# Kernel optimization log

Measured on AMD Instinct MI355X. Metric: run time of the kernel, lower is better.

Reference implementation:

```python
import jax, jax.numpy as jnp
import numpy as np

N = 2048
INPUT_DIM = 256
OUTPUT_DIM = 512
NUM_HEADS = 8
HEAD_DIM = OUTPUT_DIM // NUM_HEADS


def _lin_init(key, fan_in, fan_out):
    # torch nn.Linear default init: U(-1/sqrt(fan_in), 1/sqrt(fan_in))
    kw, kb = jax.random.split(key)
    bound = 1.0 / np.sqrt(fan_in)
    W = jax.random.uniform(kw, (fan_in, fan_out), jnp.float32, -bound, bound)
    b = jax.random.uniform(kb, (fan_out,), jnp.float32, -bound, bound)
    return W, b


def setup_inputs() -> dict:
    key = jax.random.key(0)
    ks = jax.random.split(key, 12)
    x = jax.random.normal(ks[0], (N, INPUT_DIM), jnp.float32)
    rel_pos = jax.random.normal(ks[1], (N, 2), jnp.float32)
    rel_vel = jax.random.normal(ks[2], (N, 1), jnp.float32)
    rel_angle = jax.random.normal(ks[3], (N, 1), jnp.float32)
    Wq, bq = _lin_init(ks[4], INPUT_DIM, OUTPUT_DIM)
    Wk, bk = _lin_init(ks[5], INPUT_DIM, OUTPUT_DIM)
    Wv, bv = _lin_init(ks[6], INPUT_DIM, OUTPUT_DIM)
    Wsb1, bsb1 = _lin_init(ks[7], 2, HEAD_DIM)
    Wsb2, bsb2 = _lin_init(ks[8], HEAD_DIM, 1)
    Wmg1, bmg1 = _lin_init(ks[9], 2, HEAD_DIM)
    Wmg2, bmg2 = _lin_init(ks[10], HEAD_DIM, 1)
    Wo, bo = _lin_init(ks[11], OUTPUT_DIM, 1)
    return dict(x=x, rel_pos=rel_pos, rel_vel=rel_vel, rel_angle=rel_angle,
                Wq=Wq, bq=bq, Wk=Wk, bk=bk, Wv=Wv, bv=bv,
                Wsb1=Wsb1, bsb1=bsb1, Wsb2=Wsb2, bsb2=bsb2,
                Wmg1=Wmg1, bmg1=bmg1, Wmg2=Wmg2, bmg2=bmg2,
                Wo=Wo, bo=bo)


def reference(x, rel_pos, rel_vel, rel_angle,
              Wq, bq, Wk, bk, Wv, bv,
              Wsb1, bsb1, Wsb2, bsb2,
              Wmg1, bmg1, Wmg2, bmg2,
              Wo, bo):
    n = x.shape[0]
    Q = (x @ Wq + bq).reshape(n, NUM_HEADS, HEAD_DIM)
    K = (x @ Wk + bk).reshape(n, NUM_HEADS, HEAD_DIM)
    V = (x @ Wv + bv).reshape(n, NUM_HEADS, HEAD_DIM)

    # scores[q, k, h] = <Q[q,h], K[k,h]> / sqrt(head_dim)
    scores = jnp.einsum('qhd,khd->qkh', Q, K) / np.sqrt(HEAD_DIM).astype(np.float32)

    # spatial bias: per-query scalar, broadcast over keys and heads
    sb = (jax.nn.relu(rel_pos @ Wsb1 + bsb1) @ Wsb2 + bsb2)  # (N, 1)
    scores = scores + sb[:, :, None]  # (N,1,1) broadcast -> (N,N,H)

    # softmax over key dim (dim=1)
    attention = jax.nn.softmax(scores, axis=1)

    # motion gate: per-key scalar in (0,1)
    motion_feat = jnp.concatenate([rel_vel, rel_angle], axis=-1)  # (N, 2)
    mg = jax.nn.sigmoid(jax.nn.relu(motion_feat @ Wmg1 + bmg1) @ Wmg2 + bmg2)  # (N, 1)
    attention = attention * mg[None, :, 0, None]  # (1,N,1) broadcast

    # weighted sum over keys without materializing (N,N,H,D)
    out = jnp.einsum('qkh,khd->qhd', attention, V).reshape(n, OUTPUT_DIM)
    out = out @ Wo + bo  # (N, 1)
    return out[:, 0]
```

## Files before the change

kernel.cpp:

```cpp
#include <hip/hip_runtime.h>
#include <hip/hip_bf16.h>

constexpr int N    = 2048;
constexpr int IN   = 256;
constexpr int OUT  = 512;
constexpr int NH   = 8;
constexpr int HD   = 64;
constexpr int NQK  = 1024;
constexpr int NC   = 8;
constexpr int KPB  = N / NC;
constexpr int KT   = KPB / 16;

typedef __bf16    bf16x8 __attribute__((ext_vector_type(8)));
typedef __bf16    bf16x4 __attribute__((ext_vector_type(4)));
typedef _Float16  f16x8  __attribute__((ext_vector_type(8)));
typedef float     f32x4  __attribute__((ext_vector_type(4)));

#if __has_builtin(__builtin_amdgcn_exp2f)
#define EXP2(x) __builtin_amdgcn_exp2f(x)
#else
#define EXP2(x) exp2f(x)
#endif

#define QSCALE (0.125f * 1.44269504088896f)

__global__ __launch_bounds__(256)
void prep_all(const float* __restrict__ x,
              const float* __restrict__ Wq, const float* __restrict__ Wk,
              const float* __restrict__ Wv, const float* __restrict__ bv,
              const float* __restrict__ Wo,
              __bf16* __restrict__ Xhi, __bf16* __restrict__ Xlo,
              __bf16* __restrict__ WThi, __bf16* __restrict__ WTlo,
              float* __restrict__ Wvo, float* __restrict__ bvo) {
    __shared__ float smem[32 * 33];
    const int b = blockIdx.x;
    const int tid = threadIdx.x;

    if (b < 512) {
        const size_t i4 = ((size_t)b * 256 + tid) * 4;
        const float4 v = *(const float4*)(x + i4);
        const float vv[4] = {v.x, v.y, v.z, v.w};
        bf16x4 hi, lo;
        #pragma unroll
        for (int j = 0; j < 4; j++) {
            const __bf16 h = (__bf16)vv[j];
            hi[j] = h;
            lo[j] = (__bf16)(vv[j] - (float)h);
        }
        *(bf16x4*)(Xhi + i4) = hi;
        *(bf16x4*)(Xlo + i4) = lo;
    } else if (b < 768) {
        const int tb = b - 512;
        const int k0 = (tb & 7) * 32;
        const int n0 = (tb >> 3) * 32;
        const float* W = (n0 < OUT) ? Wq : Wk;
        const int nc = (n0 < OUT) ? n0 : n0 - OUT;
        {
            const int row = tid >> 3;
            const int c4  = (tid & 7) * 4;
            const float4 v = *(const float4*)(W + (size_t)(k0 + row) * OUT + nc + c4);
            smem[row * 33 + c4 + 0] = v.x;
            smem[row * 33 + c4 + 1] = v.y;
            smem[row * 33 + c4 + 2] = v.z;
            smem[row * 33 + c4 + 3] = v.w;
        }
        __syncthreads();
        {
            const int nrow = tid >> 3;
            const int k4   = (tid & 7) * 4;
            bf16x4 hi, lo;
            #pragma unroll
            for (int j = 0; j < 4; j++) {
                const float v = smem[(k4 + j) * 33 + nrow];
                const __bf16 h = (__bf16)v;
                hi[j] = h;
                lo[j] = (__bf16)(v - (float)h);
            }
            const size_t off = (size_t)(n0 + nrow) * IN + k0 + k4;
            *(bf16x4*)(WThi + off) = hi;
            *(bf16x4*)(WTlo + off) = lo;
        }
    } else {
        float* wo_s = smem;
        wo_s[tid]       = Wo[tid];
        wo_s[tid + 256] = Wo[tid + 256];
        __syncthreads();
        const int i = (b - 768) * 32 + (tid >> 3);
        const int h = tid & 7;
        const float* wr = Wv + (size_t)i * OUT + h * HD;
        float s = 0.f;
        #pragma unroll
        for (int d = 0; d < HD; d += 4) {
            const float4 v = *(const float4*)(wr + d);
            s += v.x * wo_s[h * HD + d + 0] + v.y * wo_s[h * HD + d + 1]
               + v.z * wo_s[h * HD + d + 2] + v.w * wo_s[h * HD + d + 3];
        }
        Wvo[i * NH + h] = s;
        if (b == 768 && tid < NH) {
            float sb = 0.f;
            #pragma unroll
            for (int d = 0; d < HD; d++)
                sb += bv[tid * HD + d] * wo_s[tid * HD + d];
            bvo[tid] = sb;
        }
    }
}

__global__ __launch_bounds__(256)
void gemm_qk(const __bf16* __restrict__ Xhi, const __bf16* __restrict__ Xlo,
             const __bf16* __restrict__ WThi, const __bf16* __restrict__ WTlo,
             const float* __restrict__ bq, const float* __restrict__ bk,
             _Float16* __restrict__ Qh, _Float16* __restrict__ Kh) {
    __shared__ _Float16 stage[32 * 132];
    const int tid  = threadIdx.x;
    const int lane = tid & 63;
    const int wave = tid >> 6;
    const int row16 = lane & 15;
    const int quad  = lane >> 4;
    const int mb = blockIdx.y * 32;
    const int nb0 = blockIdx.x * 128;
    const int nb = nb0 + wave * 32;

    const size_t ar[2] = {(size_t)(mb + row16) * IN, (size_t)(mb + 16 + row16) * IN};
    const size_t br[2] = {(size_t)(nb + row16) * IN, (size_t)(nb + 16 + row16) * IN};

    f32x4 acc[2][2] = {};
    for (int k0 = 0; k0 < IN; k0 += 32) {
        const int ko = k0 + quad * 8;
        bf16x8 ah[2], al[2], bh[2], bl[2];
        #pragma unroll
        for (int t = 0; t < 2; t++) {
            ah[t] = *(const bf16x8*)(Xhi + ar[t] + ko);
            al[t] = *(const bf16x8*)(Xlo + ar[t] + ko);
            bh[t] = *(const bf16x8*)(WThi + br[t] + ko);
            bl[t] = *(const bf16x8*)(WTlo + br[t] + ko);
        }
        #pragma unroll
        for (int mt = 0; mt < 2; mt++)
            #pragma unroll
            for (int nt = 0; nt < 2; nt++) {
                acc[mt][nt] = __builtin_amdgcn_mfma_f32_16x16x32_bf16(ah[mt], bh[nt], acc[mt][nt], 0, 0, 0);
                acc[mt][nt] = __builtin_amdgcn_mfma_f32_16x16x32_bf16(ah[mt], bl[nt], acc[mt][nt], 0, 0, 0);
                acc[mt][nt] = __builtin_amdgcn_mfma_f32_16x16x32_bf16(al[mt], bh[nt], acc[mt][nt], 0, 0, 0);
            }
    }

    const bool isQ = (nb0 < OUT);
    const float scale = isQ ? QSCALE : 1.0f;
    #pragma unroll
    for (int mt = 0; mt < 2; mt++)
        #pragma unroll
        for (int nt = 0; nt < 2; nt++) {
            const int nl = wave * 32 + nt * 16 + row16;
            const int np = nb0 + nl;
            const int nq = isQ ? np : np - OUT;
            const float bias = isQ ? bq[nq] : bk[nq];
            #pragma unroll
            for (int r = 0; r < 4; r++) {
                const int ml = mt * 16 + quad * 4 + r;
                stage[ml * 132 + nl] = (_Float16)((acc[mt][nt][r] + bias) * scale);
            }
        }
    __syncthreads();

    _Float16* dst = isQ ? Qh : Kh;
    const int r2   = tid >> 2;
    const int cidx = tid & 3;
    const int hl   = r2 >> 5;
    const int m    = r2 & 31;
    const int nqh  = (isQ ? nb0 : nb0 - OUT) + hl * 64;
    const int h    = nqh >> 6;
    const size_t goff = ((size_t)h * N + mb + m) * HD + cidx * 16;
    const int soff = m * 132 + hl * 64 + cidx * 16;
    *(f16x8*)(dst + goff)     = *(const f16x8*)(&stage[soff]);
    *(f16x8*)(dst + goff + 8) = *(const f16x8*)(&stage[soff + 8]);
}

__global__ __launch_bounds__(256)
void compute_vpm(const float* __restrict__ x, const float* __restrict__ rel_vel,
                 const float* __restrict__ rel_angle,
                 const float* __restrict__ Wmg1, const float* __restrict__ bmg1,
                 const float* __restrict__ Wmg2, const float* __restrict__ bmg2,
                 const float* __restrict__ Wvo, const float* __restrict__ bvo,
                 float* __restrict__ vpmT) {
    __shared__ float wvo_s[IN * NH];
    const int tid = threadIdx.x;
    #pragma unroll
    for (int i = 0; i < 8; i++) wvo_s[tid + 256 * i] = Wvo[tid + 256 * i];
    __syncthreads();

    const int k = blockIdx.x * 32 + (tid >> 3);
    const int h = tid & 7;

    const float m0 = rel_vel[k], m1 = rel_angle[k];
    float g = bmg2[0];
    #pragma unroll
    for (int j = 0; j < HD; j++) {
        float t = m0 * Wmg1[j] + m1 * Wmg1[HD + j] + bmg1[j];
        t = fmaxf(t, 0.f);
        g += t * Wmg2[j];
    }
    const float mg = 1.f / (1.f + __expf(-g));

    const float4* xr = (const float4*)(x + (size_t)k * IN);
    float a0 = 0.f, a1 = 0.f, a2 = 0.f, a3 = 0.f;
    #pragma unroll 4
    for (int i = 0; i < IN / 4; i++) {
        const float4 v = xr[i];
        a0 += v.x * wvo_s[(i * 4 + 0) * NH + h];
        a1 += v.y * wvo_s[(i * 4 + 1) * NH + h];
        a2 += v.z * wvo_s[(i * 4 + 2) * NH + h];
        a3 += v.w * wvo_s[(i * 4 + 3) * NH + h];
    }
    vpmT[h * N + k] = mg * (a0 + a1 + a2 + a3 + bvo[h]);
}

__global__ __launch_bounds__(256)
void attn_mfma(const _Float16* __restrict__ Qh, const _Float16* __restrict__ Kh,
               const float* __restrict__ vpmT,
               float* __restrict__ pnum, float* __restrict__ pden) {
    const int b = blockIdx.x;
    const int h = b & 7;
    const int r = b >> 3;
    const int c = r >> 3;
    const int qg = r & 7;
    const int lane = threadIdx.x & 63;
    const int wave = threadIdx.x >> 6;
    const int q0 = (qg * 4 + wave) * 64;
    const int row16 = lane & 15;
    const int quad  = lane >> 4;

    f16x8 Bq[4][2];
    #pragma unroll
    for (int qt = 0; qt < 4; qt++) {
        const size_t qoff = ((size_t)h * N + q0 + qt * 16 + row16) * HD + quad * 8;
        Bq[qt][0] = *(const f16x8*)(Qh + qoff);
        Bq[qt][1] = *(const f16x8*)(Qh + qoff + 32);
    }

    float num[4] = {}, den[4] = {};
    const int k0 = c * KPB;
    const size_t kbase = ((size_t)h * N + k0 + row16) * HD + quad * 8;
    const float* vp = vpmT + h * N + k0 + quad * 4;

    f16x8 A0 = *(const f16x8*)(Kh + kbase);
    f16x8 A1 = *(const f16x8*)(Kh + kbase + 32);
    f32x4 vv = *(const f32x4*)(vp);

    #pragma unroll
    for (int t = 0; t < KT; t++) {
        const int tn = (t + 1 < KT) ? t + 1 : t;
        const size_t ka = kbase + (size_t)tn * 16 * HD;
        const f16x8 nA0 = *(const f16x8*)(Kh + ka);
        const f16x8 nA1 = *(const f16x8*)(Kh + ka + 32);
        const f32x4 nvv = *(const f32x4*)(vp + tn * 16);

        #pragma unroll
        for (int qt = 0; qt < 4; qt++) {
            f32x4 s = {0.f, 0.f, 0.f, 0.f};
            s = __builtin_amdgcn_mfma_f32_16x16x32_f16(A0, Bq[qt][0], s, 0, 0, 0);
            s = __builtin_amdgcn_mfma_f32_16x16x32_f16(A1, Bq[qt][1], s, 0, 0, 0);
            #pragma unroll
            for (int r4 = 0; r4 < 4; r4++) {
                const float e = EXP2(s[r4]);
                num[qt] += e * vv[r4];
                den[qt] += e;
            }
        }
        A0 = nA0; A1 = nA1; vv = nvv;
    }

    #pragma unroll
    for (int qt = 0; qt < 4; qt++) {
        float n = num[qt], d = den[qt];
        n += __shfl_xor(n, 16, 64);  d += __shfl_xor(d, 16, 64);
        n += __shfl_xor(n, 32, 64);  d += __shfl_xor(d, 32, 64);
        if (quad == 0) {
            const int q = q0 + qt * 16 + row16;
            pnum[((size_t)c * NH + h) * N + q] = n;
            pden[((size_t)c * NH + h) * N + q] = d;
        }
    }
}

__global__ __launch_bounds__(64)
void finalize(const float* __restrict__ pnum, const float* __restrict__ pden,
              const float* __restrict__ bo, float* __restrict__ out) {
    const int q = blockIdx.x * 64 + threadIdx.x;
    float acc = bo[0];
    #pragma unroll
    for (int h = 0; h < NH; h++) {
        float num = 0.f, den = 0.f;
        #pragma unroll
        for (int ci = 0; ci < NC; ci++) {
            num += pnum[((size_t)ci * NH + h) * N + q];
            den += pden[((size_t)ci * NH + h) * N + q];
        }
        acc += num / den;
    }
    out[q] = acc;
}

extern "C" void kernel_launch(void* const* d_in, const int* in_sizes, int n_in,
                              void* d_out, int out_size, void* d_ws, size_t ws_size,
                              hipStream_t stream) {
    const float* x         = (const float*)d_in[0];
    const float* rel_vel   = (const float*)d_in[2];
    const float* rel_angle = (const float*)d_in[3];
    const float* Wq        = (const float*)d_in[4];
    const float* bq        = (const float*)d_in[5];
    const float* Wk        = (const float*)d_in[6];
    const float* bk        = (const float*)d_in[7];
    const float* Wv        = (const float*)d_in[8];
    const float* bv        = (const float*)d_in[9];
    const float* Wmg1      = (const float*)d_in[14];
    const float* bmg1      = (const float*)d_in[15];
    const float* Wmg2      = (const float*)d_in[16];
    const float* bmg2      = (const float*)d_in[17];
    const float* Wo        = (const float*)d_in[18];
    const float* bo        = (const float*)d_in[19];
    float* out = (float*)d_out;

    __bf16* Xhi  = (__bf16*)d_ws;
    __bf16* Xlo  = Xhi + (size_t)N * IN;
    __bf16* WThi = Xlo + (size_t)N * IN;
    __bf16* WTlo = WThi + (size_t)NQK * IN;
    _Float16* Qh = (_Float16*)(WTlo + (size_t)NQK * IN);
    _Float16* Kh = Qh + (size_t)NH * N * HD;
    float* fp    = (float*)(Kh + (size_t)NH * N * HD);
    float* Wvo   = fp;
    float* bvo   = Wvo + IN * NH;
    float* vpmT  = bvo + NH;
    float* pnum  = vpmT + NH * N;
    float* pden  = pnum + (size_t)NC * NH * N;

    hipLaunchKernelGGL(prep_all, dim3(776), dim3(256), 0, stream,
                       x, Wq, Wk, Wv, bv, Wo, Xhi, Xlo, WThi, WTlo, Wvo, bvo);
    hipLaunchKernelGGL(gemm_qk, dim3(NQK / 128, N / 32), dim3(256), 0, stream,
                       Xhi, Xlo, WThi, WTlo, bq, bk, Qh, Kh);
    hipLaunchKernelGGL(compute_vpm, dim3(N / 32), dim3(256), 0, stream,
                       x, rel_vel, rel_angle, Wmg1, bmg1, Wmg2, bmg2, Wvo, bvo, vpmT);
    hipLaunchKernelGGL(attn_mfma, dim3(512), dim3(256), 0, stream,
                       Qh, Kh, vpmT, pnum, pden);
    hipLaunchKernelGGL(finalize, dim3(N / 64), dim3(64), 0, stream, pnum, pden, bo, out);
}
```

Baseline: 147.5 us.

## Use single fp16 QK projection, merge vpm into gemm, split keys into more chunks

Replaces the split-bf16 (hi/lo, three MFMAs) QK projection with a single fp16 conversion and one f16 MFMA per tile, halving the conversion traffic and cutting matrix work to a third. Folds the compute_vpm kernel into the gemm launch as extra blocks to remove a kernel launch. Doubles the key-chunk count for attention so twice as many blocks run. This costs some precision in the Q/K scores and more partial results for finalize to reduce.

After: 136.5 us. 7.5% less time.

```diff
diff --git a/kernel.cpp b/kernel.cpp
--- a/kernel.cpp
+++ b/kernel.cpp
@@ -7,13 +7,12 @@
 constexpr int NH   = 8;
 constexpr int HD   = 64;
 constexpr int NQK  = 1024;
-constexpr int NC   = 8;
+constexpr int NC   = 16;
 constexpr int KPB  = N / NC;
 constexpr int KT   = KPB / 16;
 
-typedef __bf16    bf16x8 __attribute__((ext_vector_type(8)));
-typedef __bf16    bf16x4 __attribute__((ext_vector_type(4)));
 typedef _Float16  f16x8  __attribute__((ext_vector_type(8)));
+typedef _Float16  f16x4  __attribute__((ext_vector_type(4)));
 typedef float     f32x4  __attribute__((ext_vector_type(4)));
 
 #if __has_builtin(__builtin_amdgcn_exp2f)
@@ -29,8 +28,7 @@
               const float* __restrict__ Wq, const float* __restrict__ Wk,
               const float* __restrict__ Wv, const float* __restrict__ bv,
               const float* __restrict__ Wo,
-              __bf16* __restrict__ Xhi, __bf16* __restrict__ Xlo,
-              __bf16* __restrict__ WThi, __bf16* __restrict__ WTlo,
+              _Float16* __restrict__ X16, _Float16* __restrict__ WT,
               float* __restrict__ Wvo, float* __restrict__ bvo) {
     __shared__ float smem[32 * 33];
     const int b = blockIdx.x;
@@ -39,16 +37,10 @@
     if (b < 512) {
         const size_t i4 = ((size_t)b * 256 + tid) * 4;
         const float4 v = *(const float4*)(x + i4);
-        const float vv[4] = {v.x, v.y, v.z, v.w};
-        bf16x4 hi, lo;
-        #pragma unroll
-        for (int j = 0; j < 4; j++) {
-            const __bf16 h = (__bf16)vv[j];
-            hi[j] = h;
-            lo[j] = (__bf16)(vv[j] - (float)h);
-        }
-        *(bf16x4*)(Xhi + i4) = hi;
-        *(bf16x4*)(Xlo + i4) = lo;
+        f16x4 o;
+        o[0] = (_Float16)v.x; o[1] = (_Float16)v.y;
+        o[2] = (_Float16)v.z; o[3] = (_Float16)v.w;
+        *(f16x4*)(X16 + i4) = o;
     } else if (b < 768) {
         const int tb = b - 512;
         const int k0 = (tb & 7) * 32;
@@ -68,17 +60,11 @@
         {
             const int nrow = tid >> 3;
             const int k4   = (tid & 7) * 4;
-            bf16x4 hi, lo;
-            #pragma unroll
-            for (int j = 0; j < 4; j++) {
-                const float v = smem[(k4 + j) * 33 + nrow];
-                const __bf16 h = (__bf16)v;
-                hi[j] = h;
-                lo[j] = (__bf16)(v - (float)h);
-            }
-            const size_t off = (size_t)(n0 + nrow) * IN + k0 + k4;
-            *(bf16x4*)(WThi + off) = hi;
-            *(bf16x4*)(WTlo + off) = lo;
+            f16x4 o;
+            #pragma unroll
+            for (int j = 0; j < 4; j++)
+                o[j] = (_Float16)smem[(k4 + j) * 33 + nrow];
+            *(f16x4*)(WT + (size_t)(n0 + nrow) * IN + k0 + k4) = o;
         }
     } else {
         float* wo_s = smem;
@@ -107,19 +93,58 @@
 }
 
 __global__ __launch_bounds__(256)
-void gemm_qk(const __bf16* __restrict__ Xhi, const __bf16* __restrict__ Xlo,
-             const __bf16* __restrict__ WThi, const __bf16* __restrict__ WTlo,
-             const float* __restrict__ bq, const float* __restrict__ bk,
-             _Float16* __restrict__ Qh, _Float16* __restrict__ Kh) {
+void gemm_qk_vpm(const _Float16* __restrict__ X16, const _Float16* __restrict__ WT,
+                 const float* __restrict__ bq, const float* __restrict__ bk,
+                 _Float16* __restrict__ Qh, _Float16* __restrict__ Kh,
+                 const float* __restrict__ x, const float* __restrict__ rel_vel,
+                 const float* __restrict__ rel_angle,
+                 const float* __restrict__ Wmg1, const float* __restrict__ bmg1,
+                 const float* __restrict__ Wmg2, const float* __restrict__ bmg2,
+                 const float* __restrict__ Wvo, const float* __restrict__ bvo,
+                 float* __restrict__ vpmT) {
     __shared__ _Float16 stage[32 * 132];
-    const int tid  = threadIdx.x;
+    __shared__ float wvo_s[IN * NH];
+    const int tid = threadIdx.x;
+
+    if (blockIdx.x >= 512) {
+        #pragma unroll
+        for (int i = 0; i < 8; i++) wvo_s[tid + 256 * i] = Wvo[tid + 256 * i];
+        __syncthreads();
+
+        const int k = (blockIdx.x - 512) * 32 + (tid >> 3);
+        const int h = tid & 7;
+
+        const float m0 = rel_vel[k], m1 = rel_angle[k];
+        float g = bmg2[0];
+        #pragma unroll
+        for (int j = 0; j < HD; j++) {
+            float t = m0 * Wmg1[j] + m1 * Wmg1[HD + j] + bmg1[j];
+            t = fmaxf(t, 0.f);
+            g += t * Wmg2[j];
+        }
+        const float mg = 1.f / (1.f + __expf(-g));
+
+        const float4* xr = (const float4*)(x + (size_t)k * IN);
+        float a0 = 0.f, a1 = 0.f, a2 = 0.f, a3 = 0.f;
+        #pragma unroll 4
+        for (int i = 0; i < IN / 4; i++) {
+            const float4 v = xr[i];
+            a0 += v.x * wvo_s[(i * 4 + 0) * NH + h];
+            a1 += v.y * wvo_s[(i * 4 + 1) * NH + h];
+            a2 += v.z * wvo_s[(i * 4 + 2) * NH + h];
+            a3 += v.w * wvo_s[(i * 4 + 3) * NH + h];
+        }
+        vpmT[h * N + k] = mg * (a0 + a1 + a2 + a3 + bvo[h]);
+        return;
+    }
+
     const int lane = tid & 63;
     const int wave = tid >> 6;
     const int row16 = lane & 15;
     const int quad  = lane >> 4;
-    const int mb = blockIdx.y * 32;
-    const int nb0 = blockIdx.x * 128;
-    const int nb = nb0 + wave * 32;
+    const int nb0 = (blockIdx.x & 7) * 128;
+    const int mb  = (blockIdx.x >> 3) * 32;
+    const int nb  = nb0 + wave * 32;
 
     const size_t ar[2] = {(size_t)(mb + row16) * IN, (size_t)(mb + 16 + row16) * IN};
     const size_t br[2] = {(size_t)(nb + row16) * IN, (size_t)(nb + 16 + row16) * IN};
@@ -127,22 +152,17 @@
     f32x4 acc[2][2] = {};
     for (int k0 = 0; k0 < IN; k0 += 32) {
         const int ko = k0 + quad * 8;
-        bf16x8 ah[2], al[2], bh[2], bl[2];
+        f16x8 a[2], bf[2];
         #pragma unroll
         for (int t = 0; t < 2; t++) {
-            ah[t] = *(const bf16x8*)(Xhi + ar[t] + ko);
-            al[t] = *(const bf16x8*)(Xlo + ar[t] + ko);
-            bh[t] = *(const bf16x8*)(WThi + br[t] + ko);
-            bl[t] = *(const bf16x8*)(WTlo + br[t] + ko);
+            a[t]  = *(const f16x8*)(X16 + ar[t] + ko);
+            bf[t] = *(const f16x8*)(WT + br[t] + ko);
         }
         #pragma unroll
         for (int mt = 0; mt < 2; mt++)
             #pragma unroll
-            for (int nt = 0; nt < 2; nt++) {
-                acc[mt][nt] = __builtin_amdgcn_mfma_f32_16x16x32_bf16(ah[mt], bh[nt], acc[mt][nt], 0, 0, 0);
-                acc[mt][nt] = __builtin_amdgcn_mfma_f32_16x16x32_bf16(ah[mt], bl[nt], acc[mt][nt], 0, 0, 0);
-                acc[mt][nt] = __builtin_amdgcn_mfma_f32_16x16x32_bf16(al[mt], bh[nt], acc[mt][nt], 0, 0, 0);
-            }
+            for (int nt = 0; nt < 2; nt++)
+                acc[mt][nt] = __builtin_amdgcn_mfma_f32_16x16x32_f16(a[mt], bf[nt], acc[mt][nt], 0, 0, 0);
     }
 
     const bool isQ = (nb0 < OUT);
@@ -174,45 +194,6 @@
     const int soff = m * 132 + hl * 64 + cidx * 16;
     *(f16x8*)(dst + goff)     = *(const f16x8*)(&stage[soff]);
     *(f16x8*)(dst + goff + 8) = *(const f16x8*)(&stage[soff + 8]);
-}
-
-__global__ __launch_bounds__(256)
-void compute_vpm(const float* __restrict__ x, const float* __restrict__ rel_vel,
-                 const float* __restrict__ rel_angle,
-                 const float* __restrict__ Wmg1, const float* __restrict__ bmg1,
-                 const float* __restrict__ Wmg2, const float* __restrict__ bmg2,
-                 const float* __restrict__ Wvo, const float* __restrict__ bvo,
-                 float* __restrict__ vpmT) {
-    __shared__ float wvo_s[IN * NH];
-    const int tid = threadIdx.x;
-    #pragma unroll
-    for (int i = 0; i < 8; i++) wvo_s[tid + 256 * i] = Wvo[tid + 256 * i];
-    __syncthreads();
-
-    const int k = blockIdx.x * 32 + (tid >> 3);
-    const int h = tid & 7;
-
-    const float m0 = rel_vel[k], m1 = rel_angle[k];
-    float g = bmg2[0];
-    #pragma unroll
-    for (int j = 0; j < HD; j++) {
-        float t = m0 * Wmg1[j] + m1 * Wmg1[HD + j] + bmg1[j];
-        t = fmaxf(t, 0.f);
-        g += t * Wmg2[j];
-    }
-    const float mg = 1.f / (1.f + __expf(-g));
-
-    const float4* xr = (const float4*)(x + (size_t)k * IN);
-    float a0 = 0.f, a1 = 0.f, a2 = 0.f, a3 = 0.f;
-    #pragma unroll 4
-    for (int i = 0; i < IN / 4; i++) {
-        const float4 v = xr[i];
-        a0 += v.x * wvo_s[(i * 4 + 0) * NH + h];
-        a1 += v.y * wvo_s[(i * 4 + 1) * NH + h];
-        a2 += v.z * wvo_s[(i * 4 + 2) * NH + h];
-        a3 += v.w * wvo_s[(i * 4 + 3) * NH + h];
-    }
-    vpmT[h * N + k] = mg * (a0 + a1 + a2 + a3 + bvo[h]);
 }
 
 __global__ __launch_bounds__(256)
@@ -321,26 +302,23 @@
     const float* bo        = (const float*)d_in[19];
     float* out = (float*)d_out;
 
-    __bf16* Xhi  = (__bf16*)d_ws;
-    __bf16* Xlo  = Xhi + (size_t)N * IN;
-    __bf16* WThi = Xlo + (size_t)N * IN;
-    __bf16* WTlo = WThi + (size_t)NQK * IN;
-    _Float16* Qh = (_Float16*)(WTlo + (size_t)NQK * IN);
-    _Float16* Kh = Qh + (size_t)NH * N * HD;
-    float* fp    = (float*)(Kh + (size_t)NH * N * HD);
-    float* Wvo   = fp;
-    float* bvo   = Wvo + IN * NH;
-    float* vpmT  = bvo + NH;
-    float* pnum  = vpmT + NH * N;
-    float* pden  = pnum + (size_t)NC * NH * N;
+    _Float16* X16 = (_Float16*)d_ws;
+    _Float16* WT  = X16 + (size_t)N * IN;
+    _Float16* Qh  = WT + (size_t)NQK * IN;
+    _Float16* Kh  = Qh + (size_t)NH * N * HD;
+    float* fp     = (float*)(Kh + (size_t)NH * N * HD);
+    float* Wvo    = fp;
+    float* bvo    = Wvo + IN * NH;
+    float* vpmT   = bvo + NH;
+    float* pnum   = vpmT + NH * N;
+    float* pden   = pnum + (size_t)NC * NH * N;
 
     hipLaunchKernelGGL(prep_all, dim3(776), dim3(256), 0, stream,
-                       x, Wq, Wk, Wv, bv, Wo, Xhi, Xlo, WThi, WTlo, Wvo, bvo);
-    hipLaunchKernelGGL(gemm_qk, dim3(NQK / 128, N / 32), dim3(256), 0, stream,
-                       Xhi, Xlo, WThi, WTlo, bq, bk, Qh, Kh);
-    hipLaunchKernelGGL(compute_vpm, dim3(N / 32), dim3(256), 0, stream,
+                       x, Wq, Wk, Wv, bv, Wo, X16, WT, Wvo, bvo);
+    hipLaunchKernelGGL(gemm_qk_vpm, dim3(576), dim3(256), 0, stream,
+                       X16, WT, bq, bk, Qh, Kh,
                        x, rel_vel, rel_angle, Wmg1, bmg1, Wmg2, bmg2, Wvo, bvo, vpmT);
-    hipLaunchKernelGGL(attn_mfma, dim3(512), dim3(256), 0, stream,
+    hipLaunchKernelGGL(attn_mfma, dim3(1024), dim3(256), 0, stream,
                        Qh, Kh, vpmT, pnum, pden);
     hipLaunchKernelGGL(finalize, dim3(N / 64), dim3(64), 0, stream, pnum, pden, bo, out);
 }
```
